# Performance work log

Hardware: AMD Instinct MI355X
Metric: run time of the kernel (lower is better)

Reference implementation:

```python
import jax, jax.numpy as jnp
import numpy as np

B, TK, H = 32, 8192, 256

def setup_inputs() -> dict:
    key = jax.random.key(0)
    ks = jax.random.split(key, 10)
    s = 0.02
    return {
        "s_t_hat": jax.random.normal(ks[0], (B, 2 * H), dtype=jnp.float32),
        "encoder_outputs": jax.random.normal(ks[1], (B, TK, H), dtype=jnp.float32),
        "enc_padding_mask": jnp.ones((B, TK), dtype=jnp.float32),
        "coverage": jax.random.uniform(ks[2], (B, TK), dtype=jnp.float32),
        "attn_dist_node_to_token": jax.random.uniform(ks[3], (B, TK), dtype=jnp.float32),
        "We": jax.random.normal(ks[4], (H, H), dtype=jnp.float32) * s,   # encode_proj weight
        "Wd": jax.random.normal(ks[5], (H, 2 * H), dtype=jnp.float32) * s,  # decode_proj weight
        "bd": jax.random.normal(ks[6], (H,), dtype=jnp.float32) * s,     # decode_proj bias
        "wc": jax.random.normal(ks[7], (H,), dtype=jnp.float32) * s,     # W_c weight (Linear(1,H))
        "v": jax.random.normal(ks[8], (H,), dtype=jnp.float32) * s,      # v weight (Linear(H,1))
    }

def reference(s_t_hat, encoder_outputs, enc_padding_mask, coverage,
              attn_dist_node_to_token, We, Wd, bd, wc, v):
    # encoder projection: [b,t,h] @ We^T -> [b,t,h]
    enc_feat = jnp.einsum('bth,gh->btg', encoder_outputs, We)
    # decoder projection: [b,2h] @ Wd^T + bd -> [b,h]
    dec_fea = s_t_hat @ Wd.T + bd
    # coverage feature: outer product coverage[b,t] x wc[h]
    att_features = enc_feat + dec_fea[:, None, :] + coverage[..., None] * wc
    e = jnp.tanh(att_features)
    scores = jnp.einsum('bth,h->bt', e, v)  # [b, t_k]
    attn_ = jax.nn.softmax(scores, axis=1) * enc_padding_mask
    attn = attn_ / jnp.sum(attn_, axis=1, keepdims=True)
    c_t = jnp.einsum('bt,bth->bh', attn, encoder_outputs)  # context
    new_cov = jnp.clip(coverage + attn, 0.0, 1.0)
    return (c_t, attn, new_cov)
```

## Files before the change

### kernel.cpp

```cpp
#include <hip/hip_runtime.h>

#define B_  32
#define TK_ 8192
#define H_  256
#define MT  64
#define NXB 128

typedef __bf16 bf16_t;
typedef __bf16 bf16x4 __attribute__((ext_vector_type(4)));
typedef __bf16 bf16x8 __attribute__((ext_vector_type(8)));
typedef float  floatx4 __attribute__((ext_vector_type(4)));

__device__ __forceinline__ float tanh_fast(float x) {
    float e = __builtin_amdgcn_exp2f(x * 2.885390081777927f);
    return 1.0f - 2.0f * __builtin_amdgcn_rcpf(e + 1.0f);
}

__global__ void prep_kernel(const float* __restrict__ s_t_hat,
                            const float* __restrict__ We,
                            const float* __restrict__ Wd,
                            const float* __restrict__ bd,
                            bf16_t* __restrict__ We_bf,
                            float* __restrict__ dec_ws) {
    int tid = threadIdx.x, blk = blockIdx.x;
    int gid = blk * 256 + tid;
    We_bf[gid] = (bf16_t)We[gid];

    if (blk >= 32 && blk < 160) {
        int idx  = (blk - 32) * 256 + tid;
        int pair = idx >> 2, q = idx & 3;
        int b = pair >> 8, i = pair & 255;
        const float4* sp = (const float4*)(s_t_hat + b * 2 * H_ + q * 128);
        const float4* wp = (const float4*)(Wd + (size_t)i * 2 * H_ + q * 128);
        float sum = 0.f;
        #pragma unroll 8
        for (int ii = 0; ii < 32; ++ii) {
            float4 a = sp[ii], w = wp[ii];
            sum += a.x * w.x + a.y * w.y + a.z * w.z + a.w * w.w;
        }
        sum += __shfl_xor(sum, 1, 64);
        sum += __shfl_xor(sum, 2, 64);
        if (q == 0) dec_ws[pair] = sum + bd[i];
    }
}

__global__ __launch_bounds__(256, 3) void attn_main(
    const float* __restrict__ enc,
    const float* __restrict__ mask,
    const float* __restrict__ cov,
    const float* __restrict__ wc,
    const float* __restrict__ v,
    const bf16_t* __restrict__ We_bf,
    const float* __restrict__ dec_ws,
    float* __restrict__ ctx_part,
    float* __restrict__ D_part,
    float* __restrict__ attn_out) {

    __shared__ __align__(16) bf16_t As[MT * 264];
    __shared__ float dec_s[256], wc_s[256], v_s[256];
    __shared__ float cov_s[64], mask_s[64], wexp[64];
    __shared__ float sp[4][64];
    __shared__ float ctxp[4][256];

    const int tid  = threadIdx.x;
    const int b    = blockIdx.y;
    const int xb   = blockIdx.x;
    const int t0   = xb * MT;
    const int lane = tid & 63, w = tid >> 6;
    const int l15  = lane & 15, l4 = lane >> 4;

    dec_s[tid] = dec_ws[b * 256 + tid];
    wc_s[tid]  = wc[tid];
    v_s[tid]   = v[tid];
    if (tid < 64)       cov_s[tid]       = cov[(size_t)b * TK_ + t0 + tid];
    else if (tid < 128) mask_s[tid - 64] = mask[(size_t)b * TK_ + t0 + tid - 64];

    const float* encb = enc + ((size_t)b * TK_ + t0) * H_;
    #pragma unroll
    for (int it = 0; it < 16; ++it) {
        int row = it * 4 + w;
        int h   = lane * 4;
        float4 f = *(const float4*)(encb + (size_t)row * H_ + h);
        bf16x4 p;
        p[0] = (bf16_t)f.x; p[1] = (bf16_t)f.y; p[2] = (bf16_t)f.z; p[3] = (bf16_t)f.w;
        *(bf16x4*)(&As[row * 264 + h]) = p;
    }
    __syncthreads();

    floatx4 acc[4][4];
    #pragma unroll
    for (int mi = 0; mi < 4; ++mi)
        #pragma unroll
        for (int ni = 0; ni < 4; ++ni)
            acc[mi][ni] = (floatx4){0.f, 0.f, 0.f, 0.f};

    const int wbase = w * 64;
    #pragma unroll
    for (int ks = 0; ks < 8; ++ks) {
        int k = ks * 32 + l4 * 8;
        bf16x8 a[4], bq[4];
        #pragma unroll
        for (int mi = 0; mi < 4; ++mi)
            a[mi] = *(const bf16x8*)(&As[(mi * 16 + l15) * 264 + k]);
        #pragma unroll
        for (int ni = 0; ni < 4; ++ni)
            bq[ni] = *(const bf16x8*)(We_bf + (size_t)(wbase + ni * 16 + l15) * 256 + k);
        #pragma unroll
        for (int mi = 0; mi < 4; ++mi)
            #pragma unroll
            for (int ni = 0; ni < 4; ++ni)
                acc[mi][ni] = __builtin_amdgcn_mfma_f32_16x16x32_bf16(
                    a[mi], bq[ni], acc[mi][ni], 0, 0, 0);
    }

    float decv[4], wcv[4], vv[4];
    #pragma unroll
    for (int ni = 0; ni < 4; ++ni) {
        int g = wbase + ni * 16 + l15;
        decv[ni] = dec_s[g]; wcv[ni] = wc_s[g]; vv[ni] = v_s[g];
    }
    #pragma unroll
    for (int mi = 0; mi < 4; ++mi) {
        #pragma unroll
        for (int r = 0; r < 4; ++r) {
            int t = mi * 16 + l4 * 4 + r;
            float cv = cov_s[t];
            float s = 0.f;
            #pragma unroll
            for (int ni = 0; ni < 4; ++ni) {
                float af = acc[mi][ni][r] + decv[ni] + cv * wcv[ni];
                s += tanh_fast(af) * vv[ni];
            }
            s += __shfl_xor(s, 1, 64);
            s += __shfl_xor(s, 2, 64);
            s += __shfl_xor(s, 4, 64);
            s += __shfl_xor(s, 8, 64);
            if (l15 == 0) sp[w][t] = s;
        }
    }
    __syncthreads();

    if (tid < 64) {
        int t = tid;
        float sc = sp[0][t] + sp[1][t] + sp[2][t] + sp[3][t];
        float wv = __builtin_amdgcn_exp2f(sc * 1.4426950408889634f) * mask_s[t];
        wexp[t] = wv;
        attn_out[(size_t)b * TK_ + t0 + t] = wv;
        float d = wv;
        d += __shfl_xor(d, 1, 64);  d += __shfl_xor(d, 2, 64);
        d += __shfl_xor(d, 4, 64);  d += __shfl_xor(d, 8, 64);
        d += __shfl_xor(d, 16, 64); d += __shfl_xor(d, 32, 64);
        if (tid == 0) D_part[b * NXB + xb] = d;
    }
    __syncthreads();

    {
        int h0 = lane * 4;
        float c0 = 0, c1 = 0, c2 = 0, c3 = 0;
        #pragma unroll
        for (int tt = 0; tt < 16; ++tt) {
            int t = w * 16 + tt;
            float wv = wexp[t];
            bf16x4 q = *(const bf16x4*)(&As[t * 264 + h0]);
            c0 += wv * (float)q[0];
            c1 += wv * (float)q[1];
            c2 += wv * (float)q[2];
            c3 += wv * (float)q[3];
        }
        ctxp[w][h0 + 0] = c0; ctxp[w][h0 + 1] = c1;
        ctxp[w][h0 + 2] = c2; ctxp[w][h0 + 3] = c3;
    }
    __syncthreads();
    {
        float s = ctxp[0][tid] + ctxp[1][tid] + ctxp[2][tid] + ctxp[3][tid];
        ctx_part[((size_t)b * NXB + xb) * H_ + tid] = s;
    }
}

__global__ void finalize_kernel(const float* __restrict__ cov,
                                const float* __restrict__ ctx_part,
                                const float* __restrict__ D_part,
                                float* __restrict__ out) {
    __shared__ float red[4];
    int b = blockIdx.y, chunk = blockIdx.x, tid = threadIdx.x;
    int lane = tid & 63, w = tid >> 6;

    float dv = (tid < NXB) ? D_part[b * NXB + tid] : 0.f;
    dv += __shfl_xor(dv, 1, 64);  dv += __shfl_xor(dv, 2, 64);
    dv += __shfl_xor(dv, 4, 64);  dv += __shfl_xor(dv, 8, 64);
    dv += __shfl_xor(dv, 16, 64); dv += __shfl_xor(dv, 32, 64);
    if (lane == 0) red[w] = dv;
    __syncthreads();
    float invD = 1.0f / (red[0] + red[1] + red[2] + red[3]);

    int idx = chunk * 256 + tid;
    size_t gi = (size_t)b * TK_ + idx;
    float* attn = out + 8192;
    float* ncov = out + 8192 + (size_t)B_ * TK_;
    float a = attn[gi] * invD;
    attn[gi] = a;
    float nc = cov[gi] + a;
    ncov[gi] = fminf(fmaxf(nc, 0.f), 1.f);

    if (chunk == 0) {
        const float* cp = ctx_part + (size_t)b * NXB * H_ + tid;
        float s = 0.f;
        #pragma unroll 8
        for (int x = 0; x < NXB; ++x) s += cp[(size_t)x * H_];
        out[b * 256 + tid] = s * invD;
    }
}

extern "C" void kernel_launch(void* const* d_in, const int* in_sizes, int n_in,
                              void* d_out, int out_size, void* d_ws, size_t ws_size,
                              hipStream_t stream) {
    const float* s_t_hat = (const float*)d_in[0];
    const float* enc     = (const float*)d_in[1];
    const float* mask    = (const float*)d_in[2];
    const float* cov     = (const float*)d_in[3];
    const float* We      = (const float*)d_in[5];
    const float* Wd      = (const float*)d_in[6];
    const float* bd      = (const float*)d_in[7];
    const float* wc      = (const float*)d_in[8];
    const float* v       = (const float*)d_in[9];
    float* out = (float*)d_out;

    char* ws = (char*)d_ws;
    bf16_t* We_bf   = (bf16_t*)ws;
    float*  dec_ws  = (float*)(ws + 131072);
    float*  D_part  = (float*)(ws + 131072 + 32768);
    float*  ctx_part= (float*)(ws + 131072 + 32768 + 16384);

    prep_kernel<<<256, 256, 0, stream>>>(s_t_hat, We, Wd, bd, We_bf, dec_ws);
    attn_main<<<dim3(NXB, 32), 256, 0, stream>>>(enc, mask, cov, wc, v, We_bf,
                                                 dec_ws, ctx_part, D_part, out + 8192);
    finalize_kernel<<<dim3(32, 32), 256, 0, stream>>>(cov, ctx_part, D_part, out);
}
```

Baseline: 435.9 us.

## Make attention blocks persistent over 8 sub-tiles with double-buffered encoder staging

Each block now walks 8 sub-tiles of 32 timesteps instead of handling one 64-row tile. The next sub-tile's encoder rows are prefetched into registers while the current one runs its MFMAs and softmax, then written to the other of two LDS buffers. This cuts the grid from 4096 to 1024 blocks and shrinks the partial-sum arrays that finalize must reduce, aiming to hide global load latency behind compute. The cost is fewer blocks in flight, more register pressure from the prefetch buffer, extra barriers per sub-tile, and exp and mask values recomputed by every wave.

```diff
diff --git a/kernel.cpp b/kernel.cpp
--- a/kernel.cpp
+++ b/kernel.cpp
@@ -3,8 +3,9 @@
 #define B_  32
 #define TK_ 8192
 #define H_  256
-#define MT  64
-#define NXB 128
+#define SR  32
+#define NS  8
+#define NBX 32
 
 typedef __bf16 bf16_t;
 typedef __bf16 bf16x4 __attribute__((ext_vector_type(4)));
@@ -44,7 +45,7 @@
     }
 }
 
-__global__ __launch_bounds__(256, 3) void attn_main(
+__global__ __launch_bounds__(256, 4) void attn_main(
     const float* __restrict__ enc,
     const float* __restrict__ mask,
     const float* __restrict__ cov,
@@ -56,142 +57,161 @@
     float* __restrict__ D_part,
     float* __restrict__ attn_out) {
 
-    __shared__ __align__(16) bf16_t As[MT * 264];
-    __shared__ float dec_s[256], wc_s[256], v_s[256];
-    __shared__ float cov_s[64], mask_s[64], wexp[64];
-    __shared__ float sp[4][64];
+    __shared__ __align__(16) bf16_t As[2][SR * 264];
+    __shared__ float sp[4][SR];
     __shared__ float ctxp[4][256];
 
     const int tid  = threadIdx.x;
     const int b    = blockIdx.y;
     const int xb   = blockIdx.x;
-    const int t0   = xb * MT;
     const int lane = tid & 63, w = tid >> 6;
     const int l15  = lane & 15, l4 = lane >> 4;
-
-    dec_s[tid] = dec_ws[b * 256 + tid];
-    wc_s[tid]  = wc[tid];
-    v_s[tid]   = v[tid];
-    if (tid < 64)       cov_s[tid]       = cov[(size_t)b * TK_ + t0 + tid];
-    else if (tid < 128) mask_s[tid - 64] = mask[(size_t)b * TK_ + t0 + tid - 64];
-
-    const float* encb = enc + ((size_t)b * TK_ + t0) * H_;
-    #pragma unroll
-    for (int it = 0; it < 16; ++it) {
-        int row = it * 4 + w;
-        int h   = lane * 4;
-        float4 f = *(const float4*)(encb + (size_t)row * H_ + h);
-        bf16x4 p;
-        p[0] = (bf16_t)f.x; p[1] = (bf16_t)f.y; p[2] = (bf16_t)f.z; p[3] = (bf16_t)f.w;
-        *(bf16x4*)(&As[row * 264 + h]) = p;
-    }
-    __syncthreads();
-
-    floatx4 acc[4][4];
-    #pragma unroll
-    for (int mi = 0; mi < 4; ++mi)
-        #pragma unroll
-        for (int ni = 0; ni < 4; ++ni)
-            acc[mi][ni] = (floatx4){0.f, 0.f, 0.f, 0.f};
+    const int t0b  = xb * (NS * SR);
 
     const int wbase = w * 64;
-    #pragma unroll
-    for (int ks = 0; ks < 8; ++ks) {
-        int k = ks * 32 + l4 * 8;
-        bf16x8 a[4], bq[4];
-        #pragma unroll
-        for (int mi = 0; mi < 4; ++mi)
-            a[mi] = *(const bf16x8*)(&As[(mi * 16 + l15) * 264 + k]);
-        #pragma unroll
-        for (int ni = 0; ni < 4; ++ni)
-            bq[ni] = *(const bf16x8*)(We_bf + (size_t)(wbase + ni * 16 + l15) * 256 + k);
-        #pragma unroll
-        for (int mi = 0; mi < 4; ++mi)
-            #pragma unroll
-            for (int ni = 0; ni < 4; ++ni)
-                acc[mi][ni] = __builtin_amdgcn_mfma_f32_16x16x32_bf16(
-                    a[mi], bq[ni], acc[mi][ni], 0, 0, 0);
-    }
-
     float decv[4], wcv[4], vv[4];
     #pragma unroll
     for (int ni = 0; ni < 4; ++ni) {
         int g = wbase + ni * 16 + l15;
-        decv[ni] = dec_s[g]; wcv[ni] = wc_s[g]; vv[ni] = v_s[g];
-    }
+        decv[ni] = dec_ws[b * H_ + g];
+        wcv[ni]  = wc[g];
+        vv[ni]   = v[g];
+    }
+
+    const float* encb = enc + ((size_t)b * TK_ + t0b) * H_;
+    const int colh = lane * 4;
+
     #pragma unroll
-    for (int mi = 0; mi < 4; ++mi) {
-        #pragma unroll
-        for (int r = 0; r < 4; ++r) {
-            int t = mi * 16 + l4 * 4 + r;
-            float cv = cov_s[t];
-            float s = 0.f;
+    for (int it = 0; it < 8; ++it) {
+        int row = it * 4 + w;
+        float4 f = *(const float4*)(encb + (size_t)row * H_ + colh);
+        bf16x4 q; q[0]=(bf16_t)f.x; q[1]=(bf16_t)f.y; q[2]=(bf16_t)f.z; q[3]=(bf16_t)f.w;
+        *(bf16x4*)(&As[0][row * 264 + colh]) = q;
+    }
+    __syncthreads();
+
+    float c0=0.f, c1=0.f, c2=0.f, c3=0.f;
+    float d_tot = 0.f;
+    int p = 0;
+
+    for (int s = 0; s < NS; ++s) {
+        const int tg0 = t0b + s * SR;
+
+        float4 hold[8];
+        if (s < NS - 1) {
+            const float* nb = encb + (size_t)(s + 1) * SR * H_;
+            #pragma unroll
+            for (int it = 0; it < 8; ++it) {
+                int row = it * 4 + w;
+                hold[it] = *(const float4*)(nb + (size_t)row * H_ + colh);
+            }
+        }
+
+        floatx4 acc[2][4];
+        #pragma unroll
+        for (int mi = 0; mi < 2; ++mi)
+            #pragma unroll
+            for (int ni = 0; ni < 4; ++ni)
+                acc[mi][ni] = (floatx4){0.f, 0.f, 0.f, 0.f};
+
+        #pragma unroll
+        for (int ks = 0; ks < 8; ++ks) {
+            const int k = ks * 32 + l4 * 8;
+            bf16x8 a0 = *(const bf16x8*)(&As[p][(     l15) * 264 + k]);
+            bf16x8 a1 = *(const bf16x8*)(&As[p][(16 + l15) * 264 + k]);
+            bf16x8 bq[4];
+            #pragma unroll
+            for (int ni = 0; ni < 4; ++ni)
+                bq[ni] = *(const bf16x8*)(We_bf + (size_t)(wbase + ni * 16 + l15) * H_ + k);
             #pragma unroll
             for (int ni = 0; ni < 4; ++ni) {
-                float af = acc[mi][ni][r] + decv[ni] + cv * wcv[ni];
-                s += tanh_fast(af) * vv[ni];
-            }
-            s += __shfl_xor(s, 1, 64);
-            s += __shfl_xor(s, 2, 64);
-            s += __shfl_xor(s, 4, 64);
-            s += __shfl_xor(s, 8, 64);
-            if (l15 == 0) sp[w][t] = s;
-        }
-    }
-    __syncthreads();
-
-    if (tid < 64) {
-        int t = tid;
-        float sc = sp[0][t] + sp[1][t] + sp[2][t] + sp[3][t];
-        float wv = __builtin_amdgcn_exp2f(sc * 1.4426950408889634f) * mask_s[t];
-        wexp[t] = wv;
-        attn_out[(size_t)b * TK_ + t0 + t] = wv;
-        float d = wv;
-        d += __shfl_xor(d, 1, 64);  d += __shfl_xor(d, 2, 64);
-        d += __shfl_xor(d, 4, 64);  d += __shfl_xor(d, 8, 64);
-        d += __shfl_xor(d, 16, 64); d += __shfl_xor(d, 32, 64);
-        if (tid == 0) D_part[b * NXB + xb] = d;
-    }
-    __syncthreads();
-
-    {
-        int h0 = lane * 4;
-        float c0 = 0, c1 = 0, c2 = 0, c3 = 0;
-        #pragma unroll
-        for (int tt = 0; tt < 16; ++tt) {
-            int t = w * 16 + tt;
-            float wv = wexp[t];
-            bf16x4 q = *(const bf16x4*)(&As[t * 264 + h0]);
+                acc[0][ni] = __builtin_amdgcn_mfma_f32_16x16x32_bf16(a0, bq[ni], acc[0][ni], 0, 0, 0);
+                acc[1][ni] = __builtin_amdgcn_mfma_f32_16x16x32_bf16(a1, bq[ni], acc[1][ni], 0, 0, 0);
+            }
+        }
+
+        #pragma unroll
+        for (int mi = 0; mi < 2; ++mi) {
+            #pragma unroll
+            for (int r = 0; r < 4; ++r) {
+                int tl = mi * 16 + l4 * 4 + r;
+                float cv = cov[(size_t)b * TK_ + tg0 + tl];
+                float ssum = 0.f;
+                #pragma unroll
+                for (int ni = 0; ni < 4; ++ni) {
+                    float af = acc[mi][ni][r] + decv[ni] + cv * wcv[ni];
+                    ssum += tanh_fast(af) * vv[ni];
+                }
+                ssum += __shfl_xor(ssum, 1, 64);
+                ssum += __shfl_xor(ssum, 2, 64);
+                ssum += __shfl_xor(ssum, 4, 64);
+                ssum += __shfl_xor(ssum, 8, 64);
+                if (l15 == 0) sp[w][tl] = ssum;
+            }
+        }
+        __syncthreads();
+
+        if (w == 0) {
+            float wv = 0.f;
+            if (lane < SR) {
+                float sc = sp[0][lane] + sp[1][lane] + sp[2][lane] + sp[3][lane];
+                wv = __builtin_amdgcn_exp2f(sc * 1.4426950408889634f)
+                     * mask[(size_t)b * TK_ + tg0 + lane];
+                attn_out[(size_t)b * TK_ + tg0 + lane] = wv;
+            }
+            float d = wv;
+            d += __shfl_xor(d, 1, 64);  d += __shfl_xor(d, 2, 64);
+            d += __shfl_xor(d, 4, 64);  d += __shfl_xor(d, 8, 64);
+            d += __shfl_xor(d, 16, 64); d += __shfl_xor(d, 32, 64);
+            d_tot += d;
+        }
+
+        #pragma unroll
+        for (int j = 0; j < 8; ++j) {
+            int t = w * 8 + j;
+            float sc = sp[0][t] + sp[1][t] + sp[2][t] + sp[3][t];
+            float wv = __builtin_amdgcn_exp2f(sc * 1.4426950408889634f)
+                       * mask[(size_t)b * TK_ + tg0 + t];
+            bf16x4 q = *(const bf16x4*)(&As[p][t * 264 + colh]);
             c0 += wv * (float)q[0];
             c1 += wv * (float)q[1];
             c2 += wv * (float)q[2];
             c3 += wv * (float)q[3];
         }
-        ctxp[w][h0 + 0] = c0; ctxp[w][h0 + 1] = c1;
-        ctxp[w][h0 + 2] = c2; ctxp[w][h0 + 3] = c3;
-    }
+
+        if (s < NS - 1) {
+            #pragma unroll
+            for (int it = 0; it < 8; ++it) {
+                int row = it * 4 + w;
+                float4 f = hold[it];
+                bf16x4 q; q[0]=(bf16_t)f.x; q[1]=(bf16_t)f.y; q[2]=(bf16_t)f.z; q[3]=(bf16_t)f.w;
+                *(bf16x4*)(&As[p ^ 1][row * 264 + colh]) = q;
+            }
+        }
+        __syncthreads();
+        p ^= 1;
+    }
+
+    *(float4*)(&ctxp[w][colh]) = (float4){c0, c1, c2, c3};
     __syncthreads();
-    {
-        float s = ctxp[0][tid] + ctxp[1][tid] + ctxp[2][tid] + ctxp[3][tid];
-        ctx_part[((size_t)b * NXB + xb) * H_ + tid] = s;
-    }
+    float sctx = ctxp[0][tid] + ctxp[1][tid] + ctxp[2][tid] + ctxp[3][tid];
+    ctx_part[((size_t)b * NBX + xb) * H_ + tid] = sctx;
+
+    if (w == 0 && lane == 0) D_part[b * NBX + xb] = d_tot;
 }
 
 __global__ void finalize_kernel(const float* __restrict__ cov,
                                 const float* __restrict__ ctx_part,
                                 const float* __restrict__ D_part,
                                 float* __restrict__ out) {
-    __shared__ float red[4];
     int b = blockIdx.y, chunk = blockIdx.x, tid = threadIdx.x;
-    int lane = tid & 63, w = tid >> 6;
-
-    float dv = (tid < NXB) ? D_part[b * NXB + tid] : 0.f;
+    int lane = tid & 63;
+
+    float dv = (lane < NBX) ? D_part[b * NBX + lane] : 0.f;
     dv += __shfl_xor(dv, 1, 64);  dv += __shfl_xor(dv, 2, 64);
     dv += __shfl_xor(dv, 4, 64);  dv += __shfl_xor(dv, 8, 64);
     dv += __shfl_xor(dv, 16, 64); dv += __shfl_xor(dv, 32, 64);
-    if (lane == 0) red[w] = dv;
-    __syncthreads();
-    float invD = 1.0f / (red[0] + red[1] + red[2] + red[3]);
+    float invD = 1.0f / dv;
 
     int idx = chunk * 256 + tid;
     size_t gi = (size_t)b * TK_ + idx;
@@ -203,10 +223,10 @@
     ncov[gi] = fminf(fmaxf(nc, 0.f), 1.f);
 
     if (chunk == 0) {
-        const float* cp = ctx_part + (size_t)b * NXB * H_ + tid;
+        const float* cp = ctx_part + (size_t)b * NBX * H_ + tid;
         float s = 0.f;
-        #pragma unroll 8
-        for (int x = 0; x < NXB; ++x) s += cp[(size_t)x * H_];
+        #pragma unroll
+        for (int x = 0; x < NBX; ++x) s += cp[(size_t)x * H_];
         out[b * 256 + tid] = s * invD;
     }
 }
@@ -226,13 +246,13 @@
     float* out = (float*)d_out;
 
     char* ws = (char*)d_ws;
-    bf16_t* We_bf   = (bf16_t*)ws;
-    float*  dec_ws  = (float*)(ws + 131072);
-    float*  D_part  = (float*)(ws + 131072 + 32768);
-    float*  ctx_part= (float*)(ws + 131072 + 32768 + 16384);
+    bf16_t* We_bf    = (bf16_t*)ws;
+    float*  dec_ws   = (float*)(ws + 131072);
+    float*  D_part   = (float*)(ws + 131072 + 32768);
+    float*  ctx_part = (float*)(ws + 131072 + 32768 + 4096);
 
     prep_kernel<<<256, 256, 0, stream>>>(s_t_hat, We, Wd, bd, We_bf, dec_ws);
-    attn_main<<<dim3(NXB, 32), 256, 0, stream>>>(enc, mask, cov, wc, v, We_bf,
+    attn_main<<<dim3(NBX, 32), 256, 0, stream>>>(enc, mask, cov, wc, v, We_bf,
                                                  dec_ws, ctx_part, D_part, out + 8192);
     finalize_kernel<<<dim3(32, 32), 256, 0, stream>>>(cov, ctx_part, D_part, out);
 }
```

Measured after the change: 566.1 us. +29.9%, slower.
